# Kernel optimization log

Measured on AMD Instinct MI355X. Metric: run time of the kernel, lower is better.

The kernel has to match this reference:

```python
import jax, jax.numpy as jnp
import numpy as np

EPS_RMS = 1e-8
EPS_Q = 1e-5


def rms_norm(x, scale):
    # full RMSNorm (p=-1): rms = ||x||_2 / sqrt(d); y = scale * x / (rms + eps)
    d = x.shape[-1]
    norm = jnp.linalg.norm(x, axis=-1, keepdims=True)
    rms = norm * (d ** -0.5)
    return scale * (x / (rms + EPS_RMS))


def activation_quant(x):
    # per-token int8 abs-max quant
    s = 127.0 / jnp.clip(jnp.max(jnp.abs(x), axis=-1, keepdims=True), EPS_Q, None)
    return jnp.clip(jnp.round(x * s), -128, 127) / s


def weight_quant(w):
    # per-tensor ternary abs-mean quant
    s = 1.0 / jnp.clip(jnp.mean(jnp.abs(w)), EPS_Q, None)
    return jnp.clip(jnp.round(w * s), -1, 1) / s


def bit_linear(x, w, scale):
    x_q = activation_quant(rms_norm(x, scale))  # forward value of STE
    w_q = weight_quant(w)
    return x_q @ w_q.T


def setup_inputs() -> dict:
    key = jax.random.key(0)
    ks = jax.random.split(key, 4)
    B = 65536
    x = jax.random.normal(ks[0], (B, 784), dtype=jnp.float32)
    w1 = jax.random.normal(ks[1], (128, 784), dtype=jnp.float32) * (784 ** -0.5)
    w2 = jax.random.normal(ks[2], (64, 128), dtype=jnp.float32) * (128 ** -0.5)
    w3 = jax.random.normal(ks[3], (10, 64), dtype=jnp.float32) * (64 ** -0.5)
    return {
        'x': x,
        'w1': w1, 'scale1': jnp.ones((784,), jnp.float32),
        'w2': w2, 'scale2': jnp.ones((128,), jnp.float32),
        'w3': w3, 'scale3': jnp.ones((64,), jnp.float32),
    }


def reference(x, w1, scale1, w2, scale2, w3, scale3):
    h = jax.nn.relu(bit_linear(x, w1, scale1))
    h = jax.nn.relu(bit_linear(h, w2, scale2))
    return bit_linear(h, w3, scale3)
```

## Files before the change

### kernel.cpp

```cpp
#include <hip/hip_runtime.h>
#include <stdint.h>


typedef int   ix4 __attribute__((ext_vector_type(4)));
typedef float fx4 __attribute__((ext_vector_type(4)));

#define MFMA_I8(a, b, c) __builtin_amdgcn_mfma_i32_16x16x64_i8((a), (b), (c), 0, 0, 0)

__device__ __forceinline__ void sync_lds() {
  asm volatile("s_waitcnt lgkmcnt(0)" ::: "memory");
  __builtin_amdgcn_s_barrier();
}
__device__ __forceinline__ void wave_lds_fence() {
  asm volatile("s_waitcnt lgkmcnt(0)" ::: "memory");
}

__global__ __launch_bounds__(256) void prep_mean(
    const float* __restrict__ w1, const float* __restrict__ w2,
    const float* __restrict__ w3, double* __restrict__ sums) {
  __shared__ double red[256];
  const int b = blockIdx.x;
  const float* w; int n, nb, bb, which;
  if (b < 240)      { w = w1; n = 128 * 784; nb = 240; bb = b;       which = 0; }
  else if (b < 248) { w = w2; n = 64 * 128;  nb = 8;   bb = b - 240; which = 1; }
  else              { w = w3; n = 10 * 64;   nb = 1;   bb = 0;       which = 2; }
  double s = 0.0;
  for (int i = bb * 256 + (int)threadIdx.x; i < n; i += nb * 256)
    s += (double)fabsf(w[i]);
  red[threadIdx.x] = s;
  __syncthreads();
  for (int off = 128; off > 0; off >>= 1) {
    if ((int)threadIdx.x < off) red[threadIdx.x] += red[threadIdx.x + off];
    __syncthreads();
  }
  if (threadIdx.x == 0) atomicAdd(&sums[which], red[0]);
}

__global__ __launch_bounds__(256) void prep_quant(
    const float* __restrict__ w1, const float* __restrict__ w2,
    const float* __restrict__ w3, const double* __restrict__ sums,
    int8_t* __restrict__ t1, int8_t* __restrict__ t2,
    int8_t* __restrict__ t3p) {
  const int idx = blockIdx.x * 256 + (int)threadIdx.x;
  const float s1 = 1.0f / fmaxf((float)(sums[0] * (1.0 / (128.0 * 784.0))), 1e-5f);
  const float s2 = 1.0f / fmaxf((float)(sums[1] * (1.0 / (64.0 * 128.0))), 1e-5f);
  const float s3 = 1.0f / fmaxf((float)(sums[2] * (1.0 / (10.0 * 64.0))), 1e-5f);
  if (idx < 128 * 832) {
    const int n = idx / 832, k = idx - n * 832;
    float v = 0.f;
    if (k < 784) v = fminf(fmaxf(rintf(w1[n * 784 + k] * s1), -1.f), 1.f);
    t1[idx] = (int8_t)(int)v;
  } else if (idx < 128 * 832 + 64 * 128) {
    const int i = idx - 128 * 832;
    t2[i] = (int8_t)(int)fminf(fmaxf(rintf(w2[i] * s2), -1.f), 1.f);
  } else if (idx < 128 * 832 + 64 * 128 + 16 * 64) {
    const int i = idx - (128 * 832 + 64 * 128);
    const int n = i >> 6, p = i & 63;
    const int ch = (p >> 2) + 16 * (p & 3);
    float v = 0.f;
    if (n < 10) v = fminf(fmaxf(rintf(w3[n * 64 + ch] * s3), -1.f), 1.f);
    t3p[i] = (int8_t)(int)v;
  }
}

__global__ __launch_bounds__(256)
__attribute__((amdgpu_waves_per_eu(2, 4)))
void ffn_l1(
    const float* __restrict__ x,
    const float* __restrict__ sc1, const float* __restrict__ sc2,
    const int8_t* __restrict__ t1, const double* __restrict__ sums,
    int8_t* __restrict__ q2g, float* __restrict__ inv2g, int numTiles) {
  __shared__ int8_t q1[16 * 848];
  __shared__ float  h1[16 * 132];
  __shared__ float  inv1[16];

  const int tid = threadIdx.x;
  const int l   = tid & 63;
  const int wv  = tid >> 6;
  const int g   = l >> 4;
  const int sl  = l & 15;
  const int token = wv * 4 + g;

  const float m1 = fmaxf((float)(sums[0] * (1.0 / (128.0 * 784.0))), 1e-5f);

  if (tid < 192) {
    const int t = tid / 12, c = tid - (tid / 12) * 12;
    *reinterpret_cast<unsigned*>(&q1[t * 848 + 784 + c * 4]) = 0u;
  }

  fx4 xv[13];
  int tile = blockIdx.x;
  if (tile < numTiles) {
    const float* rowp = x + (size_t)(tile * 16 + token) * 784;
#pragma unroll
    for (int c = 0; c < 12; ++c)
      xv[c] = *reinterpret_cast<const fx4*>(rowp + (sl + 16 * c) * 4);
    if (sl < 4) xv[12] = *reinterpret_cast<const fx4*>(rowp + (sl + 192) * 4);
  }

  for (; tile < numTiles; tile += (int)gridDim.x) {
    float ss = 0.f, am = 0.f;
#pragma unroll
    for (int c = 0; c < 12; ++c) {
      fx4 v = xv[c];
      fx4 s4 = *reinterpret_cast<const fx4*>(sc1 + (sl + 16 * c) * 4);
      ss += v[0] * v[0] + v[1] * v[1] + v[2] * v[2] + v[3] * v[3];
      am = fmaxf(am, fmaxf(fmaxf(fabsf(v[0] * s4[0]), fabsf(v[1] * s4[1])),
                           fmaxf(fabsf(v[2] * s4[2]), fabsf(v[3] * s4[3]))));
    }
    if (sl < 4) {
      fx4 v = xv[12];
      fx4 s4 = *reinterpret_cast<const fx4*>(sc1 + (sl + 192) * 4);
      ss += v[0] * v[0] + v[1] * v[1] + v[2] * v[2] + v[3] * v[3];
      am = fmaxf(am, fmaxf(fmaxf(fabsf(v[0] * s4[0]), fabsf(v[1] * s4[1])),
                           fmaxf(fabsf(v[2] * s4[2]), fabsf(v[3] * s4[3]))));
    }
#pragma unroll
    for (int m = 1; m < 16; m <<= 1) {
      ss += __shfl_xor(ss, m, 64);
      am = fmaxf(am, __shfl_xor(am, m, 64));
    }
    const float denom = sqrtf(ss) * (1.0f / 28.0f) + 1e-8f;
    const float invd  = 1.0f / denom;
    const float cl    = fmaxf(am * invd, 1e-5f);
    const float gq    = (127.0f / cl) * invd;
    if (sl == 0) inv1[token] = cl * (1.0f / 127.0f);

#pragma unroll
    for (int c = 0; c < 12; ++c) {
      fx4 v = xv[c];
      fx4 s4 = *reinterpret_cast<const fx4*>(sc1 + (sl + 16 * c) * 4);
      int q0 = (int)fminf(fmaxf(rintf(v[0] * s4[0] * gq), -128.f), 127.f);
      int q1i = (int)fminf(fmaxf(rintf(v[1] * s4[1] * gq), -128.f), 127.f);
      int q2i = (int)fminf(fmaxf(rintf(v[2] * s4[2] * gq), -128.f), 127.f);
      int q3i = (int)fminf(fmaxf(rintf(v[3] * s4[3] * gq), -128.f), 127.f);
      unsigned p = (unsigned)(q0 & 255) | ((unsigned)(q1i & 255) << 8) |
                   ((unsigned)(q2i & 255) << 16) | ((unsigned)(q3i & 255) << 24);
      *reinterpret_cast<unsigned*>(&q1[token * 848 + (sl + 16 * c) * 4]) = p;
    }
    if (sl < 4) {
      fx4 v = xv[12];
      fx4 s4 = *reinterpret_cast<const fx4*>(sc1 + (sl + 192) * 4);
      int q0 = (int)fminf(fmaxf(rintf(v[0] * s4[0] * gq), -128.f), 127.f);
      int q1i = (int)fminf(fmaxf(rintf(v[1] * s4[1] * gq), -128.f), 127.f);
      int q2i = (int)fminf(fmaxf(rintf(v[2] * s4[2] * gq), -128.f), 127.f);
      int q3i = (int)fminf(fmaxf(rintf(v[3] * s4[3] * gq), -128.f), 127.f);
      unsigned p = (unsigned)(q0 & 255) | ((unsigned)(q1i & 255) << 8) |
                   ((unsigned)(q2i & 255) << 16) | ((unsigned)(q3i & 255) << 24);
      *reinterpret_cast<unsigned*>(&q1[token * 848 + (sl + 192) * 4]) = p;
    }

    {
      const int ntile = tile + (int)gridDim.x;
      if (ntile < numTiles) {
        const float* rowp = x + (size_t)(ntile * 16 + token) * 784;
#pragma unroll
        for (int c = 0; c < 12; ++c)
          xv[c] = *reinterpret_cast<const fx4*>(rowp + (sl + 16 * c) * 4);
        if (sl < 4) xv[12] = *reinterpret_cast<const fx4*>(rowp + (sl + 192) * 4);
      }
    }

    sync_lds();

    ix4 acc0 = {0, 0, 0, 0}, acc1 = {0, 0, 0, 0};
    {
      const int8_t* b0p = t1 + (wv * 32 + sl) * 832;
      const int8_t* b1p = b0p + 16 * 832;
#pragma unroll 4
      for (int kk = 0; kk < 13; ++kk) {
        const int k0 = kk * 64 + g * 16;
        ix4 a  = *reinterpret_cast<const ix4*>(&q1[sl * 848 + k0]);
        ix4 b0 = *reinterpret_cast<const ix4*>(b0p + k0);
        ix4 b1 = *reinterpret_cast<const ix4*>(b1p + k0);
        acc0 = MFMA_I8(a, b0, acc0);
        acc1 = MFMA_I8(a, b1, acc1);
      }
    }
#pragma unroll
    for (int r = 0; r < 4; ++r) {
      const int tr = g * 4 + r;
      const float s = inv1[tr] * m1;
      h1[tr * 132 + wv * 32 + sl]      = fmaxf((float)acc0[r] * s, 0.f);
      h1[tr * 132 + wv * 32 + 16 + sl] = fmaxf((float)acc1[r] * s, 0.f);
    }
    sync_lds();

    {
      fx4 v0 = *reinterpret_cast<const fx4*>(&h1[token * 132 + sl * 4]);
      fx4 v1 = *reinterpret_cast<const fx4*>(&h1[token * 132 + 64 + sl * 4]);
      fx4 s0 = *reinterpret_cast<const fx4*>(sc2 + sl * 4);
      fx4 s1 = *reinterpret_cast<const fx4*>(sc2 + 64 + sl * 4);
      float ss2 = v0[0]*v0[0] + v0[1]*v0[1] + v0[2]*v0[2] + v0[3]*v0[3]
                + v1[0]*v1[0] + v1[1]*v1[1] + v1[2]*v1[2] + v1[3]*v1[3];
      float am2 = fmaxf(fmaxf(fmaxf(fabsf(v0[0]*s0[0]), fabsf(v0[1]*s0[1])),
                              fmaxf(fabsf(v0[2]*s0[2]), fabsf(v0[3]*s0[3]))),
                        fmaxf(fmaxf(fabsf(v1[0]*s1[0]), fabsf(v1[1]*s1[1])),
                              fmaxf(fabsf(v1[2]*s1[2]), fabsf(v1[3]*s1[3]))));
#pragma unroll
      for (int m = 1; m < 16; m <<= 1) {
        ss2 += __shfl_xor(ss2, m, 64);
        am2 = fmaxf(am2, __shfl_xor(am2, m, 64));
      }
      const float den2 = sqrtf(ss2) * 0.08838834764831845f + 1e-8f;
      const float id2  = 1.0f / den2;
      const float cl2  = fmaxf(am2 * id2, 1e-5f);
      const float gq2  = (127.0f / cl2) * id2;
      const size_t tok = (size_t)tile * 16 + token;
      if (sl == 0) inv2g[tok] = cl2 * (1.0f / 127.0f);
      int a0 = (int)fminf(fmaxf(rintf(v0[0]*s0[0]*gq2), -128.f), 127.f);
      int a1 = (int)fminf(fmaxf(rintf(v0[1]*s0[1]*gq2), -128.f), 127.f);
      int a2 = (int)fminf(fmaxf(rintf(v0[2]*s0[2]*gq2), -128.f), 127.f);
      int a3 = (int)fminf(fmaxf(rintf(v0[3]*s0[3]*gq2), -128.f), 127.f);
      int b0 = (int)fminf(fmaxf(rintf(v1[0]*s1[0]*gq2), -128.f), 127.f);
      int b1 = (int)fminf(fmaxf(rintf(v1[1]*s1[1]*gq2), -128.f), 127.f);
      int b2 = (int)fminf(fmaxf(rintf(v1[2]*s1[2]*gq2), -128.f), 127.f);
      int b3 = (int)fminf(fmaxf(rintf(v1[3]*s1[3]*gq2), -128.f), 127.f);
      unsigned pa = (unsigned)(a0 & 255) | ((unsigned)(a1 & 255) << 8) |
                    ((unsigned)(a2 & 255) << 16) | ((unsigned)(a3 & 255) << 24);
      unsigned pb = (unsigned)(b0 & 255) | ((unsigned)(b1 & 255) << 8) |
                    ((unsigned)(b2 & 255) << 16) | ((unsigned)(b3 & 255) << 24);
      *reinterpret_cast<unsigned*>(q2g + tok * 128 + sl * 4)      = pa;
      *reinterpret_cast<unsigned*>(q2g + tok * 128 + 64 + sl * 4) = pb;
    }
  }
}

__global__ __launch_bounds__(256) void ffn_l23(
    const int8_t* __restrict__ q2g, const float* __restrict__ inv2g,
    const float* __restrict__ sc3,
    const int8_t* __restrict__ t2, const int8_t* __restrict__ t3p,
    const double* __restrict__ sums, float* __restrict__ out) {
  __shared__ int8_t wbuf[4][16 * 64];

  const int tid = threadIdx.x;
  const int l   = tid & 63;
  const int wv  = tid >> 6;
  const int g   = l >> 4;
  const int sl  = l & 15;
  const int wtok0 = (blockIdx.x * 4 + wv) * 16;

  const float m2 = fmaxf((float)(sums[1] * (1.0 / (64.0 * 128.0))), 1e-5f);
  const float m3 = fmaxf((float)(sums[2] * (1.0 / (10.0 * 64.0))), 1e-5f);

  ix4 a0 = *reinterpret_cast<const ix4*>(q2g + (size_t)(wtok0 + sl) * 128 + g * 16);
  ix4 a1 = *reinterpret_cast<const ix4*>(q2g + (size_t)(wtok0 + sl) * 128 + 64 + g * 16);
  fx4 i2 = *reinterpret_cast<const fx4*>(inv2g + wtok0 + 4 * g);

  ix4 acc[4];
#pragma unroll
  for (int nt = 0; nt < 4; ++nt) {
    ix4 c = {0, 0, 0, 0};
    const int8_t* bp = t2 + (nt * 16 + sl) * 128;
    c = MFMA_I8(a0, *reinterpret_cast<const ix4*>(bp + g * 16), c);
    c = MFMA_I8(a1, *reinterpret_cast<const ix4*>(bp + 64 + g * 16), c);
    acc[nt] = c;
  }

  float sc3v[4];
#pragma unroll
  for (int nt = 0; nt < 4; ++nt) sc3v[nt] = sc3[nt * 16 + sl];

  float h2v[4][4];
  float ss3[4] = {0.f, 0.f, 0.f, 0.f}, am3[4] = {0.f, 0.f, 0.f, 0.f};
#pragma unroll
  for (int nt = 0; nt < 4; ++nt)
#pragma unroll
    for (int r = 0; r < 4; ++r) {
      float h = fmaxf((float)acc[nt][r] * i2[r] * m2, 0.f);
      h2v[nt][r] = h;
      ss3[r] += h * h;
      am3[r] = fmaxf(am3[r], fabsf(h * sc3v[nt]));
    }
#pragma unroll
  for (int m = 1; m < 16; m <<= 1) {
#pragma unroll
    for (int r = 0; r < 4; ++r) {
      ss3[r] += __shfl_xor(ss3[r], m, 64);
      am3[r] = fmaxf(am3[r], __shfl_xor(am3[r], m, 64));
    }
  }
  float gq3[4], i3[4];
#pragma unroll
  for (int r = 0; r < 4; ++r) {
    const float den3 = sqrtf(ss3[r]) * 0.125f + 1e-8f;
    const float id3  = 1.0f / den3;
    const float cl3  = fmaxf(am3[r] * id3, 1e-5f);
    gq3[r] = (127.0f / cl3) * id3;
    i3[r]  = cl3 * (1.0f / 127.0f) * m3;
  }

#pragma unroll
  for (int r = 0; r < 4; ++r) {
    int c0 = (int)fminf(fmaxf(rintf(h2v[0][r] * sc3v[0] * gq3[r]), -128.f), 127.f);
    int c1 = (int)fminf(fmaxf(rintf(h2v[1][r] * sc3v[1] * gq3[r]), -128.f), 127.f);
    int c2 = (int)fminf(fmaxf(rintf(h2v[2][r] * sc3v[2] * gq3[r]), -128.f), 127.f);
    int c3 = (int)fminf(fmaxf(rintf(h2v[3][r] * sc3v[3] * gq3[r]), -128.f), 127.f);
    unsigned p = (unsigned)(c0 & 255) | ((unsigned)(c1 & 255) << 8) |
                 ((unsigned)(c2 & 255) << 16) | ((unsigned)(c3 & 255) << 24);
    *reinterpret_cast<unsigned*>(&wbuf[wv][(4 * g + r) * 64 + sl * 4]) = p;
  }
  wave_lds_fence();

  ix4 a3 = *reinterpret_cast<const ix4*>(&wbuf[wv][sl * 64 + g * 16]);
  ix4 b3 = *reinterpret_cast<const ix4*>(t3p + sl * 64 + g * 16);
  ix4 acc3 = {0, 0, 0, 0};
  acc3 = MFMA_I8(a3, b3, acc3);

  if (sl < 10) {
#pragma unroll
    for (int r = 0; r < 4; ++r)
      out[(size_t)(wtok0 + 4 * g + r) * 10 + sl] = (float)acc3[r] * i3[r];
  }
}

extern "C" void kernel_launch(void* const* d_in, const int* in_sizes, int n_in,
                              void* d_out, int out_size, void* d_ws, size_t ws_size,
                              hipStream_t stream) {
  const float* x  = (const float*)d_in[0];
  const float* w1 = (const float*)d_in[1];
  const float* s1 = (const float*)d_in[2];
  const float* w2 = (const float*)d_in[3];
  const float* s2 = (const float*)d_in[4];
  const float* w3 = (const float*)d_in[5];
  const float* s3 = (const float*)d_in[6];
  float* out = (float*)d_out;

  char* ws = (char*)d_ws;
  double* sums = (double*)ws;
  int8_t* t1   = (int8_t*)(ws + 1024);
  int8_t* t2   = (int8_t*)(ws + 107520);
  int8_t* t3p  = (int8_t*)(ws + 115712);
  float*  inv2 = (float*)(ws + 116736);
  int8_t* q2   = (int8_t*)(ws + 378880);

  const int B = in_sizes[0] / 784;
  const int numTiles = B / 16;

  hipMemsetAsync(sums, 0, 3 * sizeof(double), stream);
  prep_mean<<<249, 256, 0, stream>>>(w1, w2, w3, sums);
  const int total_q = 128 * 832 + 64 * 128 + 16 * 64;
  prep_quant<<<(total_q + 255) / 256, 256, 0, stream>>>(w1, w2, w3, sums, t1, t2, t3p);
  const int grid1 = numTiles < 1024 ? numTiles : 1024;
  ffn_l1<<<grid1, 256, 0, stream>>>(x, s1, s2, t1, sums, q2, inv2, numTiles);
  ffn_l23<<<B / 64, 256, 0, stream>>>(q2, inv2, s3, t2, t3p, sums, out);
}
```

Baseline: 319.5 us.

## Replace persistent prefetching L1 loop with one-tile-per-block launch and higher occupancy

Drops the persistent grid-stride loop in the first-layer kernel, which held the next tile of x in registers as a software prefetch. The kernel now launches one block per 16-token tile and re-reads x from global memory (likely L1/L2 hits) in the quantize pass instead of keeping 13 float4 registers live. The waves-per-EU hint rises to a minimum of 4 so more waves can hide memory latency. The cost is the lost explicit prefetch overlap, a second read of each row, and per-block setup and LDS-padding init repeated for 4096 blocks.

```diff
diff --git a/kernel.cpp b/kernel.cpp
--- a/kernel.cpp
+++ b/kernel.cpp
@@ -64,12 +64,12 @@
 }
 
 __global__ __launch_bounds__(256)
-__attribute__((amdgpu_waves_per_eu(2, 4)))
+__attribute__((amdgpu_waves_per_eu(4)))
 void ffn_l1(
     const float* __restrict__ x,
     const float* __restrict__ sc1, const float* __restrict__ sc2,
     const int8_t* __restrict__ t1, const double* __restrict__ sums,
-    int8_t* __restrict__ q2g, float* __restrict__ inv2g, int numTiles) {
+    int8_t* __restrict__ q2g, float* __restrict__ inv2g) {
   __shared__ int8_t q1[16 * 848];
   __shared__ float  h1[16 * 132];
   __shared__ float  inv1[16];
@@ -88,141 +88,120 @@
     *reinterpret_cast<unsigned*>(&q1[t * 848 + 784 + c * 4]) = 0u;
   }
 
-  fx4 xv[13];
-  int tile = blockIdx.x;
-  if (tile < numTiles) {
-    const float* rowp = x + (size_t)(tile * 16 + token) * 784;
-#pragma unroll
-    for (int c = 0; c < 12; ++c)
-      xv[c] = *reinterpret_cast<const fx4*>(rowp + (sl + 16 * c) * 4);
-    if (sl < 4) xv[12] = *reinterpret_cast<const fx4*>(rowp + (sl + 192) * 4);
-  }
-
-  for (; tile < numTiles; tile += (int)gridDim.x) {
-    float ss = 0.f, am = 0.f;
-#pragma unroll
-    for (int c = 0; c < 12; ++c) {
-      fx4 v = xv[c];
-      fx4 s4 = *reinterpret_cast<const fx4*>(sc1 + (sl + 16 * c) * 4);
-      ss += v[0] * v[0] + v[1] * v[1] + v[2] * v[2] + v[3] * v[3];
-      am = fmaxf(am, fmaxf(fmaxf(fabsf(v[0] * s4[0]), fabsf(v[1] * s4[1])),
-                           fmaxf(fabsf(v[2] * s4[2]), fabsf(v[3] * s4[3]))));
+  const float* rowp = x + (size_t)(blockIdx.x * 16 + token) * 784;
+
+  float ss = 0.f, am = 0.f;
+#pragma unroll
+  for (int c = 0; c < 12; ++c) {
+    fx4 v  = *reinterpret_cast<const fx4*>(rowp + (sl + 16 * c) * 4);
+    fx4 s4 = *reinterpret_cast<const fx4*>(sc1 + (sl + 16 * c) * 4);
+    ss += v[0] * v[0] + v[1] * v[1] + v[2] * v[2] + v[3] * v[3];
+    am = fmaxf(am, fmaxf(fmaxf(fabsf(v[0] * s4[0]), fabsf(v[1] * s4[1])),
+                         fmaxf(fabsf(v[2] * s4[2]), fabsf(v[3] * s4[3]))));
+  }
+  if (sl < 4) {
+    fx4 v  = *reinterpret_cast<const fx4*>(rowp + (sl + 192) * 4);
+    fx4 s4 = *reinterpret_cast<const fx4*>(sc1 + (sl + 192) * 4);
+    ss += v[0] * v[0] + v[1] * v[1] + v[2] * v[2] + v[3] * v[3];
+    am = fmaxf(am, fmaxf(fmaxf(fabsf(v[0] * s4[0]), fabsf(v[1] * s4[1])),
+                         fmaxf(fabsf(v[2] * s4[2]), fabsf(v[3] * s4[3]))));
+  }
+#pragma unroll
+  for (int m = 1; m < 16; m <<= 1) {
+    ss += __shfl_xor(ss, m, 64);
+    am = fmaxf(am, __shfl_xor(am, m, 64));
+  }
+  const float denom = sqrtf(ss) * (1.0f / 28.0f) + 1e-8f;
+  const float invd  = 1.0f / denom;
+  const float cl    = fmaxf(am * invd, 1e-5f);
+  const float gq    = (127.0f / cl) * invd;
+  if (sl == 0) inv1[token] = cl * (1.0f / 127.0f);
+
+#pragma unroll
+  for (int c = 0; c < 12; ++c) {
+    fx4 v  = *reinterpret_cast<const fx4*>(rowp + (sl + 16 * c) * 4);
+    fx4 s4 = *reinterpret_cast<const fx4*>(sc1 + (sl + 16 * c) * 4);
+    int q0  = (int)fminf(fmaxf(rintf(v[0] * s4[0] * gq), -128.f), 127.f);
+    int q1i = (int)fminf(fmaxf(rintf(v[1] * s4[1] * gq), -128.f), 127.f);
+    int q2i = (int)fminf(fmaxf(rintf(v[2] * s4[2] * gq), -128.f), 127.f);
+    int q3i = (int)fminf(fmaxf(rintf(v[3] * s4[3] * gq), -128.f), 127.f);
+    unsigned p = (unsigned)(q0 & 255) | ((unsigned)(q1i & 255) << 8) |
+                 ((unsigned)(q2i & 255) << 16) | ((unsigned)(q3i & 255) << 24);
+    *reinterpret_cast<unsigned*>(&q1[token * 848 + (sl + 16 * c) * 4]) = p;
+  }
+  if (sl < 4) {
+    fx4 v  = *reinterpret_cast<const fx4*>(rowp + (sl + 192) * 4);
+    fx4 s4 = *reinterpret_cast<const fx4*>(sc1 + (sl + 192) * 4);
+    int q0  = (int)fminf(fmaxf(rintf(v[0] * s4[0] * gq), -128.f), 127.f);
+    int q1i = (int)fminf(fmaxf(rintf(v[1] * s4[1] * gq), -128.f), 127.f);
+    int q2i = (int)fminf(fmaxf(rintf(v[2] * s4[2] * gq), -128.f), 127.f);
+    int q3i = (int)fminf(fmaxf(rintf(v[3] * s4[3] * gq), -128.f), 127.f);
+    unsigned p = (unsigned)(q0 & 255) | ((unsigned)(q1i & 255) << 8) |
+                 ((unsigned)(q2i & 255) << 16) | ((unsigned)(q3i & 255) << 24);
+    *reinterpret_cast<unsigned*>(&q1[token * 848 + (sl + 192) * 4]) = p;
+  }
+
+  sync_lds();
+
+  ix4 acc0 = {0, 0, 0, 0}, acc1 = {0, 0, 0, 0};
+  {
+    const int8_t* b0p = t1 + (wv * 32 + sl) * 832;
+    const int8_t* b1p = b0p + 16 * 832;
+#pragma unroll 4
+    for (int kk = 0; kk < 13; ++kk) {
+      const int k0 = kk * 64 + g * 16;
+      ix4 a  = *reinterpret_cast<const ix4*>(&q1[sl * 848 + k0]);
+      ix4 b0 = *reinterpret_cast<const ix4*>(b0p + k0);
+      ix4 b1 = *reinterpret_cast<const ix4*>(b1p + k0);
+      acc0 = MFMA_I8(a, b0, acc0);
+      acc1 = MFMA_I8(a, b1, acc1);
     }
-    if (sl < 4) {
-      fx4 v = xv[12];
-      fx4 s4 = *reinterpret_cast<const fx4*>(sc1 + (sl + 192) * 4);
-      ss += v[0] * v[0] + v[1] * v[1] + v[2] * v[2] + v[3] * v[3];
-      am = fmaxf(am, fmaxf(fmaxf(fabsf(v[0] * s4[0]), fabsf(v[1] * s4[1])),
-                           fmaxf(fabsf(v[2] * s4[2]), fabsf(v[3] * s4[3]))));
+  }
+#pragma unroll
+  for (int r = 0; r < 4; ++r) {
+    const int tr = g * 4 + r;
+    const float s = inv1[tr] * m1;
+    h1[tr * 132 + wv * 32 + sl]      = fmaxf((float)acc0[r] * s, 0.f);
+    h1[tr * 132 + wv * 32 + 16 + sl] = fmaxf((float)acc1[r] * s, 0.f);
+  }
+  sync_lds();
+
+  {
+    fx4 v0 = *reinterpret_cast<const fx4*>(&h1[token * 132 + sl * 4]);
+    fx4 v1 = *reinterpret_cast<const fx4*>(&h1[token * 132 + 64 + sl * 4]);
+    fx4 s0 = *reinterpret_cast<const fx4*>(sc2 + sl * 4);
+    fx4 s1 = *reinterpret_cast<const fx4*>(sc2 + 64 + sl * 4);
+    float ss2 = v0[0]*v0[0] + v0[1]*v0[1] + v0[2]*v0[2] + v0[3]*v0[3]
+              + v1[0]*v1[0] + v1[1]*v1[1] + v1[2]*v1[2] + v1[3]*v1[3];
+    float am2 = fmaxf(fmaxf(fmaxf(fabsf(v0[0]*s0[0]), fabsf(v0[1]*s0[1])),
+                            fmaxf(fabsf(v0[2]*s0[2]), fabsf(v0[3]*s0[3]))),
+                      fmaxf(fmaxf(fabsf(v1[0]*s1[0]), fabsf(v1[1]*s1[1])),
+                            fmaxf(fabsf(v1[2]*s1[2]), fabsf(v1[3]*s1[3]))));
+#pragma unroll
+    for (int m = 1; m < 16; m <<= 1) {
+      ss2 += __shfl_xor(ss2, m, 64);
+      am2 = fmaxf(am2, __shfl_xor(am2, m, 64));
     }
-#pragma unroll
-    for (int m = 1; m < 16; m <<= 1) {
-      ss += __shfl_xor(ss, m, 64);
-      am = fmaxf(am, __shfl_xor(am, m, 64));
-    }
-    const float denom = sqrtf(ss) * (1.0f / 28.0f) + 1e-8f;
-    const float invd  = 1.0f / denom;
-    const float cl    = fmaxf(am * invd, 1e-5f);
-    const float gq    = (127.0f / cl) * invd;
-    if (sl == 0) inv1[token] = cl * (1.0f / 127.0f);
-
-#pragma unroll
-    for (int c = 0; c < 12; ++c) {
-      fx4 v = xv[c];
-      fx4 s4 = *reinterpret_cast<const fx4*>(sc1 + (sl + 16 * c) * 4);
-      int q0 = (int)fminf(fmaxf(rintf(v[0] * s4[0] * gq), -128.f), 127.f);
-      int q1i = (int)fminf(fmaxf(rintf(v[1] * s4[1] * gq), -128.f), 127.f);
-      int q2i = (int)fminf(fmaxf(rintf(v[2] * s4[2] * gq), -128.f), 127.f);
-      int q3i = (int)fminf(fmaxf(rintf(v[3] * s4[3] * gq), -128.f), 127.f);
-      unsigned p = (unsigned)(q0 & 255) | ((unsigned)(q1i & 255) << 8) |
-                   ((unsigned)(q2i & 255) << 16) | ((unsigned)(q3i & 255) << 24);
-      *reinterpret_cast<unsigned*>(&q1[token * 848 + (sl + 16 * c) * 4]) = p;
-    }
-    if (sl < 4) {
-      fx4 v = xv[12];
-      fx4 s4 = *reinterpret_cast<const fx4*>(sc1 + (sl + 192) * 4);
-      int q0 = (int)fminf(fmaxf(rintf(v[0] * s4[0] * gq), -128.f), 127.f);
-      int q1i = (int)fminf(fmaxf(rintf(v[1] * s4[1] * gq), -128.f), 127.f);
-      int q2i = (int)fminf(fmaxf(rintf(v[2] * s4[2] * gq), -128.f), 127.f);
-      int q3i = (int)fminf(fmaxf(rintf(v[3] * s4[3] * gq), -128.f), 127.f);
-      unsigned p = (unsigned)(q0 & 255) | ((unsigned)(q1i & 255) << 8) |
-                   ((unsigned)(q2i & 255) << 16) | ((unsigned)(q3i & 255) << 24);
-      *reinterpret_cast<unsigned*>(&q1[token * 848 + (sl + 192) * 4]) = p;
-    }
-
-    {
-      const int ntile = tile + (int)gridDim.x;
-      if (ntile < numTiles) {
-        const float* rowp = x + (size_t)(ntile * 16 + token) * 784;
-#pragma unroll
-        for (int c = 0; c < 12; ++c)
-          xv[c] = *reinterpret_cast<const fx4*>(rowp + (sl + 16 * c) * 4);
-        if (sl < 4) xv[12] = *reinterpret_cast<const fx4*>(rowp + (sl + 192) * 4);
-      }
-    }
-
-    sync_lds();
-
-    ix4 acc0 = {0, 0, 0, 0}, acc1 = {0, 0, 0, 0};
-    {
-      const int8_t* b0p = t1 + (wv * 32 + sl) * 832;
-      const int8_t* b1p = b0p + 16 * 832;
-#pragma unroll 4
-      for (int kk = 0; kk < 13; ++kk) {
-        const int k0 = kk * 64 + g * 16;
-        ix4 a  = *reinterpret_cast<const ix4*>(&q1[sl * 848 + k0]);
-        ix4 b0 = *reinterpret_cast<const ix4*>(b0p + k0);
-        ix4 b1 = *reinterpret_cast<const ix4*>(b1p + k0);
-        acc0 = MFMA_I8(a, b0, acc0);
-        acc1 = MFMA_I8(a, b1, acc1);
-      }
-    }
-#pragma unroll
-    for (int r = 0; r < 4; ++r) {
-      const int tr = g * 4 + r;
-      const float s = inv1[tr] * m1;
-      h1[tr * 132 + wv * 32 + sl]      = fmaxf((float)acc0[r] * s, 0.f);
-      h1[tr * 132 + wv * 32 + 16 + sl] = fmaxf((float)acc1[r] * s, 0.f);
-    }
-    sync_lds();
-
-    {
-      fx4 v0 = *reinterpret_cast<const fx4*>(&h1[token * 132 + sl * 4]);
-      fx4 v1 = *reinterpret_cast<const fx4*>(&h1[token * 132 + 64 + sl * 4]);
-      fx4 s0 = *reinterpret_cast<const fx4*>(sc2 + sl * 4);
-      fx4 s1 = *reinterpret_cast<const fx4*>(sc2 + 64 + sl * 4);
-      float ss2 = v0[0]*v0[0] + v0[1]*v0[1] + v0[2]*v0[2] + v0[3]*v0[3]
-                + v1[0]*v1[0] + v1[1]*v1[1] + v1[2]*v1[2] + v1[3]*v1[3];
-      float am2 = fmaxf(fmaxf(fmaxf(fabsf(v0[0]*s0[0]), fabsf(v0[1]*s0[1])),
-                              fmaxf(fabsf(v0[2]*s0[2]), fabsf(v0[3]*s0[3]))),
-                        fmaxf(fmaxf(fabsf(v1[0]*s1[0]), fabsf(v1[1]*s1[1])),
-                              fmaxf(fabsf(v1[2]*s1[2]), fabsf(v1[3]*s1[3]))));
-#pragma unroll
-      for (int m = 1; m < 16; m <<= 1) {
-        ss2 += __shfl_xor(ss2, m, 64);
-        am2 = fmaxf(am2, __shfl_xor(am2, m, 64));
-      }
-      const float den2 = sqrtf(ss2) * 0.08838834764831845f + 1e-8f;
-      const float id2  = 1.0f / den2;
-      const float cl2  = fmaxf(am2 * id2, 1e-5f);
-      const float gq2  = (127.0f / cl2) * id2;
-      const size_t tok = (size_t)tile * 16 + token;
-      if (sl == 0) inv2g[tok] = cl2 * (1.0f / 127.0f);
-      int a0 = (int)fminf(fmaxf(rintf(v0[0]*s0[0]*gq2), -128.f), 127.f);
-      int a1 = (int)fminf(fmaxf(rintf(v0[1]*s0[1]*gq2), -128.f), 127.f);
-      int a2 = (int)fminf(fmaxf(rintf(v0[2]*s0[2]*gq2), -128.f), 127.f);
-      int a3 = (int)fminf(fmaxf(rintf(v0[3]*s0[3]*gq2), -128.f), 127.f);
-      int b0 = (int)fminf(fmaxf(rintf(v1[0]*s1[0]*gq2), -128.f), 127.f);
-      int b1 = (int)fminf(fmaxf(rintf(v1[1]*s1[1]*gq2), -128.f), 127.f);
-      int b2 = (int)fminf(fmaxf(rintf(v1[2]*s1[2]*gq2), -128.f), 127.f);
-      int b3 = (int)fminf(fmaxf(rintf(v1[3]*s1[3]*gq2), -128.f), 127.f);
-      unsigned pa = (unsigned)(a0 & 255) | ((unsigned)(a1 & 255) << 8) |
-                    ((unsigned)(a2 & 255) << 16) | ((unsigned)(a3 & 255) << 24);
-      unsigned pb = (unsigned)(b0 & 255) | ((unsigned)(b1 & 255) << 8) |
-                    ((unsigned)(b2 & 255) << 16) | ((unsigned)(b3 & 255) << 24);
-      *reinterpret_cast<unsigned*>(q2g + tok * 128 + sl * 4)      = pa;
-      *reinterpret_cast<unsigned*>(q2g + tok * 128 + 64 + sl * 4) = pb;
-    }
+    const float den2 = sqrtf(ss2) * 0.08838834764831845f + 1e-8f;
+    const float id2  = 1.0f / den2;
+    const float cl2  = fmaxf(am2 * id2, 1e-5f);
+    const float gq2  = (127.0f / cl2) * id2;
+    const size_t tok = (size_t)blockIdx.x * 16 + token;
+    if (sl == 0) inv2g[tok] = cl2 * (1.0f / 127.0f);
+    int a0 = (int)fminf(fmaxf(rintf(v0[0]*s0[0]*gq2), -128.f), 127.f);
+    int a1 = (int)fminf(fmaxf(rintf(v0[1]*s0[1]*gq2), -128.f), 127.f);
+    int a2 = (int)fminf(fmaxf(rintf(v0[2]*s0[2]*gq2), -128.f), 127.f);
+    int a3 = (int)fminf(fmaxf(rintf(v0[3]*s0[3]*gq2), -128.f), 127.f);
+    int b0 = (int)fminf(fmaxf(rintf(v1[0]*s1[0]*gq2), -128.f), 127.f);
+    int b1 = (int)fminf(fmaxf(rintf(v1[1]*s1[1]*gq2), -128.f), 127.f);
+    int b2 = (int)fminf(fmaxf(rintf(v1[2]*s1[2]*gq2), -128.f), 127.f);
+    int b3 = (int)fminf(fmaxf(rintf(v1[3]*s1[3]*gq2), -128.f), 127.f);
+    unsigned pa = (unsigned)(a0 & 255) | ((unsigned)(a1 & 255) << 8) |
+                  ((unsigned)(a2 & 255) << 16) | ((unsigned)(a3 & 255) << 24);
+    unsigned pb = (unsigned)(b0 & 255) | ((unsigned)(b1 & 255) << 8) |
+                  ((unsigned)(b2 & 255) << 16) | ((unsigned)(b3 & 255) << 24);
+    *reinterpret_cast<unsigned*>(q2g + tok * 128 + sl * 4)      = pa;
+    *reinterpret_cast<unsigned*>(q2g + tok * 128 + 64 + sl * 4) = pb;
   }
 }
 
@@ -341,7 +320,6 @@
   prep_mean<<<249, 256, 0, stream>>>(w1, w2, w3, sums);
   const int total_q = 128 * 832 + 64 * 128 + 16 * 64;
   prep_quant<<<(total_q + 255) / 256, 256, 0, stream>>>(w1, w2, w3, sums, t1, t2, t3p);
-  const int grid1 = numTiles < 1024 ? numTiles : 1024;
-  ffn_l1<<<grid1, 256, 0, stream>>>(x, s1, s2, t1, sums, q2, inv2, numTiles);
+  ffn_l1<<<numTiles, 256, 0, stream>>>(x, s1, s2, t1, sums, q2, inv2);
   ffn_l23<<<B / 64, 256, 0, stream>>>(q2, inv2, s3, t2, t3p, sums, out);
 }
```

Result: slower. 332.0 us (+3.9%).
